# Optimization experiments

Measured on AMD Instinct MI355X. Metric: run time of the kernel, lower is better.

## Reference

```python
import jax, jax.numpy as jnp
import numpy as np
from jax import lax

B, N, C = 256, 256, 192
HEADS = 6
HD = C // HEADS
WIN = 16
AGENT = 49
POOL = 7            # int(agent_num ** 0.5)
SCALE = HD ** -0.5


def _pool_matrix(inn, out):
    # PyTorch AdaptiveAvgPool2d bin edges: start=floor(i*inn/out), end=ceil((i+1)*inn/out)
    P = np.zeros((out, inn), np.float32)
    for i in range(out):
        s = (i * inn) // out
        e = -(((-(i + 1)) * inn) // out)
        P[i, s:e] = 1.0 / (e - s)
    return jnp.asarray(P)

_P = _pool_matrix(WIN, POOL)  # (7, 16) adaptive-avg-pool operator


def _resize_bilinear(x, out_h, out_w):
    # matches F.interpolate(mode='bilinear', align_corners=False)
    H, W = x.shape[-2], x.shape[-1]
    def idx(out, inn):
        s = (jnp.arange(out, dtype=jnp.float32) + 0.5) * (inn / out) - 0.5
        s = jnp.maximum(s, 0.0)
        i0 = jnp.minimum(jnp.floor(s).astype(jnp.int32), inn - 1)
        i1 = jnp.minimum(i0 + 1, inn - 1)
        return i0, i1, s - i0.astype(jnp.float32)
    h0, h1, th = idx(out_h, H)
    w0, w1, tw = idx(out_w, W)
    xh = x[..., h0, :] * (1.0 - th)[:, None] + x[..., h1, :] * th[:, None]
    return xh[..., :, w0] * (1.0 - tw) + xh[..., :, w1] * tw


def setup_inputs() -> dict:
    key = jax.random.key(0)
    ks = jax.random.split(key, 18)
    lin = lambda k: jax.random.normal(k, (C, C), jnp.float32) * 0.02
    zc = jnp.zeros((C,), jnp.float32)
    tn = lambda k, shp: jax.random.normal(k, shp, jnp.float32) * 0.02
    return {
        "x_F1": jax.random.normal(ks[0], (B, N, C), jnp.float32),
        "x_C2": jax.random.normal(ks[1], (B, N, C), jnp.float32),
        "x_C1": jax.random.normal(ks[2], (B, N, C), jnp.float32),
        "Wq": lin(ks[3]), "bq": zc,
        "Wk": lin(ks[4]), "bk": zc,
        "Wv": lin(ks[5]), "bv": zc,
        "Wa1": lin(ks[6]), "ba1": zc,
        "Wa2": lin(ks[7]), "ba2": zc,
        "an_bias": tn(ks[8], (HEADS, AGENT, 7, 7)),
        "na_bias": tn(ks[9], (HEADS, AGENT, 7, 7)),
        "ah_bias": tn(ks[10], (1, HEADS, AGENT, WIN, 1)),
        "aw_bias": tn(ks[11], (1, HEADS, AGENT, 1, WIN)),
        "ha_bias": tn(ks[12], (1, HEADS, WIN, 1, AGENT)),
        "wa_bias": tn(ks[13], (1, HEADS, 1, WIN, AGENT)),
        "dwc_w": tn(ks[14], (C, 1, 3, 3)),
        "dwc_b": zc,
        "Wp": lin(ks[15]), "bp": zc,
    }


def reference(x_F1, x_C2, x_C1, Wq, bq, Wk, bk, Wv, bv, Wa1, ba1, Wa2, ba2,
              an_bias, na_bias, ah_bias, aw_bias, ha_bias, wa_bias,
              dwc_w, dwc_b, Wp, bp):
    b, n, c = x_F1.shape
    h = w = WIN
    q = x_F1 @ Wq.T + bq
    k = (x_F1 + x_C2 - x_C1) @ Wk.T + bk
    v = (x_C2 - x_C1) @ Wv.T + bv
    # agent tokens: linear -> adaptive avg pool 16x16 -> 7x7 -> (b, 49, c)
    a1 = (x_C1 @ Wa1.T + ba1).reshape(b, h, w, c)
    a1 = jnp.einsum('ph,bhwc,qw->bpqc', _P, a1, _P).reshape(b, AGENT, c)
    a2 = (x_C2 @ Wa2.T + ba2).reshape(b, h, w, c)
    a2 = jnp.einsum('ph,bhwc,qw->bpqc', _P, a2, _P).reshape(b, AGENT, c)
    qh = q.reshape(b, n, HEADS, HD).transpose(0, 2, 1, 3)
    kh = k.reshape(b, n, HEADS, HD).transpose(0, 2, 1, 3)
    vh = v.reshape(b, n, HEADS, HD).transpose(0, 2, 1, 3)
    a1h = a1.reshape(b, AGENT, HEADS, HD).transpose(0, 2, 1, 3)
    a2h = a2.reshape(b, AGENT, HEADS, HD).transpose(0, 2, 1, 3)
    # stage 1: agent <- k/v attention, bias = interp(an_bias) + (ah+aw)
    pb = (_resize_bilinear(an_bias, h, w).reshape(1, HEADS, AGENT, n)
          + (ah_bias + aw_bias).reshape(1, HEADS, AGENT, n))
    attn2 = jax.nn.softmax(SCALE * jnp.einsum('bhad,bhnd->bhan', a2h, kh) + pb, axis=-1)
    agent_v = jnp.einsum('bhan,bhnd->bhad', attn2, vh)
    # stage 2: query <- agent attention, bias = interp(na_bias)^T + (ha+wa)
    ab = (jnp.swapaxes(_resize_bilinear(na_bias, h, w).reshape(HEADS, AGENT, n), -1, -2)[None]
          + (ha_bias + wa_bias).reshape(1, HEADS, n, AGENT))
    q_attn = jax.nn.softmax(SCALE * jnp.einsum('bhnd,bhad->bhna', qh, a1h) + ab, axis=-1)
    x = jnp.einsum('bhna,bhad->bhnd', q_attn, agent_v).transpose(0, 2, 1, 3).reshape(b, n, c)
    # depthwise 3x3 conv on q as spatial map
    q_img = q.reshape(b, h, w, c).transpose(0, 3, 1, 2)
    dw = lax.conv_general_dilated(q_img, dwc_w, (1, 1), ((1, 1), (1, 1)),
                                  feature_group_count=c,
                                  dimension_numbers=('NCHW', 'OIHW', 'NCHW'))
    dw = dw + dwc_b.reshape(1, c, 1, 1)
    x = x + dw.transpose(0, 2, 3, 1).reshape(b, n, c)
    return x @ Wp.T + bp
```

## Files before the change

kernel.cpp:

```cpp
#include <hip/hip_runtime.h>

typedef __bf16 bf16;
typedef __bf16 bf16x4 __attribute__((ext_vector_type(4)));
typedef __bf16 bf16x8 __attribute__((ext_vector_type(8)));
typedef float  f32x4  __attribute__((ext_vector_type(4)));

#define DEVI __device__ __forceinline__

static constexpr int   BATCH = 256;
static constexpr int   SEQ   = 256;
static constexpr int   CH    = 192;
static constexpr int   NH    = 6;
static constexpr int   AG    = 49;
static constexpr float QK_SCALE = 0.17677669529663687f;

__device__ constexpr int   PPN[16]  = {1,1,2,1,2,1,2,1,1,2,1,2,1,2,1,1};
__device__ constexpr int   PPB0[16] = {0,0,0,1,1,2,2,3,3,3,4,4,5,5,6,6};
__device__ constexpr int   PPB1[16] = {0,0,1,0,2,0,3,0,0,4,0,5,0,6,0,0};
__device__ constexpr float PPW0[16] = {1.f/3.f,1.f/3.f,1.f/3.f,1.f/3.f,1.f/3.f,1.f/3.f,1.f/3.f,0.25f,0.25f,0.25f,
                                       1.f/3.f,1.f/3.f,1.f/3.f,1.f/3.f,1.f/3.f,1.f/3.f};
__device__ constexpr float PPW1[16] = {0.f,0.f,1.f/3.f,0.f,1.f/3.f,0.f,0.25f,0.f,0.f,1.f/3.f,
                                       0.f,1.f/3.f,0.f,1.f/3.f,0.f,0.f};

#if defined(__has_builtin)
#if __has_builtin(__builtin_amdgcn_global_load_lds)
#define HAVE_GLL 1
#endif
#endif

DEVI void gll16(const void* g, void* l, int lane) {
#ifdef HAVE_GLL
  (void)lane;
  __builtin_amdgcn_global_load_lds(
      (const __attribute__((address_space(1))) void*)g,
      (__attribute__((address_space(3))) void*)l, 16, 0, 0);
#else
  *(uint4*)((char*)l + lane * 16) = *(const uint4*)((const char*)g);
#endif
}

DEVI float bilin7(const float* m, int i, int j) {
  float sh = (i + 0.5f) * 0.4375f - 0.5f; sh = sh < 0.f ? 0.f : sh;
  float sw = (j + 0.5f) * 0.4375f - 0.5f; sw = sw < 0.f ? 0.f : sw;
  int i0 = (int)sh; if (i0 > 6) i0 = 6;
  int j0 = (int)sw; if (j0 > 6) j0 = 6;
  int i1 = i0 + 1;  if (i1 > 6) i1 = 6;
  int j1 = j0 + 1;  if (j1 > 6) j1 = 6;
  float th = sh - (float)i0, tw = sw - (float)j0;
  float v00 = m[i0*7 + j0], v01 = m[i0*7 + j1];
  float v10 = m[i1*7 + j0], v11 = m[i1*7 + j1];
  return (v00*(1.f-tw) + v01*tw)*(1.f-th) + (v10*(1.f-tw) + v11*tw)*th;
}

__global__ void k_prep(const float* Wq, const float* Wk, const float* Wv,
                       const float* Wa1, const float* Wa2, const float* Wp,
                       const float* an_bias, const float* na_bias,
                       const float* ah_bias, const float* aw_bias,
                       const float* ha_bias, const float* wa_bias,
                       bf16* wsW, bf16* pb, bf16* ab, bf16* a1, bf16* a2) {
  int gid = blockIdx.x * 256 + threadIdx.x;
  if (gid < 221184) {
    int mi = gid / 36864, r = gid - mi * 36864;
    const float* W = (mi == 0 ? Wq : mi == 1 ? Wk : mi == 2 ? Wv :
                      mi == 3 ? Wa1 : mi == 4 ? Wa2 : Wp);
    wsW[gid] = (bf16)W[r];
  } else if (gid < 296448) {
    int r = gid - 221184;
    int n = r & 255, ha = r >> 8;
    int i = n >> 4, j = n & 15;
    float val = bilin7(an_bias + (size_t)ha * 49, i, j)
              + ah_bias[ha * 16 + i] + aw_bias[ha * 16 + j];
    pb[r] = (bf16)val;
  } else if (gid < 382464) {
    int r = gid - 296448;
    int a = r % 56, hn = r / 56;
    int n = hn & 255, hh = hn >> 8;
    int i = n >> 4, j = n & 15;
    float val = 0.f;
    if (a < AG)
      val = bilin7(na_bias + (size_t)(hh * 49 + a) * 49, i, j)
          + ha_bias[(hh * 16 + i) * 49 + a] + wa_bias[(hh * 16 + j) * 49 + a];
    ab[r] = (bf16)val;
  } else if (gid < 407040) {
    int r = gid - 382464;
    if (r < 12288) a1[(size_t)12544 * CH + r] = (bf16)0.f;
    else           a2[(size_t)12544 * CH + (r - 12288)] = (bf16)0.f;
  }
}

__global__ __launch_bounds__(256, 4) void k_combo(
    const float* xF1, const float* xC2, const float* xC1,
    bf16* f1b, bf16* kin, bf16* vin) {
  const int base = blockIdx.x * 1536 + threadIdx.x;
  #pragma unroll
  for (int g = 0; g < 2; ++g) {
    int rows[3], byts[3];
    float f[3][8], c2[3][8], c1[3][8];
    #pragma unroll
    for (int s = 0; s < 3; ++s) {
      const int slot = base + 256 * (3 * g + s);
      const int row  = slot / 24;
      const int cb   = slot - row * 24;
      rows[s] = row;
      byts[s] = (cb * 16) ^ ((row & 7) << 4);
      const size_t rf = (size_t)row * CH + cb * 8;
      *(float4*)&f[s][0]  = *(const float4*)(xF1 + rf);
      *(float4*)&f[s][4]  = *(const float4*)(xF1 + rf + 4);
      *(float4*)&c2[s][0] = *(const float4*)(xC2 + rf);
      *(float4*)&c2[s][4] = *(const float4*)(xC2 + rf + 4);
      *(float4*)&c1[s][0] = *(const float4*)(xC1 + rf);
      *(float4*)&c1[s][4] = *(const float4*)(xC1 + rf + 4);
    }
    #pragma unroll
    for (int s = 0; s < 3; ++s) {
      bf16x8 tq, tk, tv;
      #pragma unroll
      for (int e = 0; e < 8; ++e) {
        const float d = c2[s][e] - c1[s][e];
        tq[e] = (bf16)f[s][e];
        tk[e] = (bf16)(f[s][e] + d);
        tv[e] = (bf16)d;
      }
      const size_t rowb = (size_t)rows[s] * 384;
      *(bf16x8*)((char*)f1b + rowb + byts[s]) = tq;
      *(bf16x8*)((char*)kin + rowb + byts[s]) = tk;
      *(bf16x8*)((char*)vin + rowb + byts[s]) = tv;
    }
  }
}

__global__ __launch_bounds__(256, 3) void k_gemm3b(
    const bf16* f1b, const bf16* kin, const bf16* vin, const bf16* wsW,
    const float* bq, const float* bk, const float* bv,
    bf16* qO, bf16* kO, bf16* vT) {
  __shared__ char sA[49152] __attribute__((aligned(16)));
  const int tid = threadIdx.x, lane = tid & 63, wid = tid >> 6;
  const int l15 = lane & 15, lg = lane >> 4;
  const int wr = wid >> 1, wc = wid & 1;
  const int job = blockIdx.y;
  const int m0 = blockIdx.x * 128;
  const bf16*  Aj   = (job == 0 ? f1b : job == 1 ? kin : vin);
  const bf16*  Wj   = wsW + job * 36864;
  const float* bias = (job == 0 ? bq : job == 1 ? bk : bv);

  {
    const char* gsrc = (const char*)Aj + (size_t)m0 * 384;
    #pragma unroll
    for (int i = 0; i < 12; ++i) {
      const int off = (wid * 12 + i) * 1024;
      gll16(gsrc + off + lane * 16, sA + off, lane);
    }
  }
  __syncthreads();

  f32x4 acc[4][6];
  #pragma unroll
  for (int a = 0; a < 4; ++a)
    #pragma unroll
    for (int b2 = 0; b2 < 6; ++b2) acc[a][b2] = f32x4{0.f, 0.f, 0.f, 0.f};

  #pragma unroll
  for (int kk = 0; kk < 6; ++kk) {
    bf16x8 af[4];
    #pragma unroll
    for (int rt = 0; rt < 4; ++rt) {
      const int row = 64 * wr + 16 * rt + l15;
      af[rt] = *(const bf16x8*)(sA + row * 384 + ((kk * 64 + lg * 16) ^ ((row & 7) << 4)));
    }
    #pragma unroll
    for (int ct = 0; ct < 6; ++ct) {
      const int ncol = 96 * wc + 16 * ct + l15;
      bf16x8 bfr = *(const bf16x8*)&Wj[(size_t)ncol * CH + kk * 32 + 8 * lg];
      #pragma unroll
      for (int rt = 0; rt < 4; ++rt)
        acc[rt][ct] = __builtin_amdgcn_mfma_f32_16x16x32_bf16(af[rt], bfr, acc[rt][ct], 0, 0, 0);
    }
  }
  __syncthreads();

  if (job < 2) {
    bf16* outp = (job == 0 ? qO : kO);
    #pragma unroll
    for (int ct = 0; ct < 6; ++ct) {
      const int col = 96 * wc + 16 * ct + l15;
      const float bb = bias[col];
      #pragma unroll
      for (int rt = 0; rt < 4; ++rt)
        #pragma unroll
        for (int r = 0; r < 4; ++r) {
          const int row = 64 * wr + 16 * rt + 4 * lg + r;
          *(bf16*)(sA + row * 384 + ((2 * col) ^ ((row & 7) << 4))) = (bf16)(acc[rt][ct][r] + bb);
        }
    }
    __syncthreads();
    #pragma unroll
    for (int g = 0; g < 12; ++g) {
      const int ch  = tid + 256 * g;
      const int row = ch / 24;
      const int y   = (ch - row * 24) * 16;
      bf16x8 vv = *(const bf16x8*)(sA + row * 384 + (y ^ ((row & 7) << 4)));
      *(bf16x8*)((char*)outp + (size_t)(m0 + row) * 384 + y) = vv;
    }
  } else {
    #pragma unroll
    for (int ct = 0; ct < 6; ++ct) {
      const int col = 96 * wc + 16 * ct + l15;
      const float bb = bias[col];
      #pragma unroll
      for (int rt = 0; rt < 4; ++rt)
        #pragma unroll
        for (int r = 0; r < 4; ++r) {
          const int row = 64 * wr + 16 * rt + 4 * lg + r;
          const int byt = col * 256 + (((2 * row) & ~15) ^ ((col & 7) << 4)) + ((2 * row) & 15);
          *(bf16*)(sA + byt) = (bf16)(acc[rt][ct][r] + bb);
        }
    }
    __syncthreads();
    const int batch = m0 >> 8, nb = m0 & 255;
    #pragma unroll
    for (int g = 0; g < 12; ++g) {
      const int ch = tid + 256 * g;
      const int c = ch >> 4, o = ch & 15;
      bf16x8 vv = *(const bf16x8*)(sA + c * 256 + ((o * 16) ^ ((c & 7) << 4)));
      *(bf16x8*)(vT + (((size_t)batch * NH + (c >> 5)) * 32 + (c & 31)) * 256 + nb + 8 * o) = vv;
    }
  }
}

#define POOLROW(I, P0, W0, P1, W1) do {                                        \
    float jqx[7] = {0,0,0,0,0,0,0}, jqy[7] = {0,0,0,0,0,0,0};                  \
    _Pragma("unroll")                                                          \
    for (int j = 0; j < 16; ++j) {                                             \
      float2 x = *(const float2*)(src + (size_t)((I) * 16 + j) * CH);          \
      jqx[PPB0[j]] += PPW0[j] * x.x;  jqy[PPB0[j]] += PPW0[j] * x.y;           \
      if (PPN[j] == 2) { jqx[PPB1[j]] += PPW1[j] * x.x;                        \
                         jqy[PPB1[j]] += PPW1[j] * x.y; }                      \
    }                                                                          \
    _Pragma("unroll")                                                          \
    for (int q = 0; q < 7; ++q) { ax[P0][q] += (W0) * jqx[q];                  \
                                  ay[P0][q] += (W0) * jqy[q]; }                \
    if ((P1) >= 0) {                                                           \
      _Pragma("unroll")                                                        \
      for (int q = 0; q < 7; ++q) { ax[(P1) & 3][q] += (W1) * jqx[q];          \
                                    ay[(P1) & 3][q] += (W1) * jqy[q]; }        \
    }                                                                          \
  } while (0)

__global__ __launch_bounds__(192) void k_pool(
    const float* xC1, const float* xC2, bf16* pooled1, bf16* pooled2) {
  __shared__ float lred[7][192];
  const int b = blockIdx.x, which = blockIdx.y, t = threadIdx.x;
  const int cp = t % 96, ih = t / 96;
  const float* src = (which ? xC2 : xC1) + (size_t)b * SEQ * CH + 2 * cp;
  bf16* dst = (which ? pooled2 : pooled1) + (size_t)b * AG * CH + 2 * cp;

  float ax[4][7], ay[4][7];
  #pragma unroll
  for (int p = 0; p < 4; ++p)
    #pragma unroll
    for (int q = 0; q < 7; ++q) { ax[p][q] = 0.f; ay[p][q] = 0.f; }

  const float TH = 1.f / 3.f, QU = 0.25f;
  if (ih == 0) {
    POOLROW(0, 0, TH, -1, 0.f);  POOLROW(1, 0, TH, -1, 0.f);
    POOLROW(2, 0, TH,  1, TH);   POOLROW(3, 1, TH, -1, 0.f);
    POOLROW(4, 1, TH,  2, TH);   POOLROW(5, 2, TH, -1, 0.f);
    POOLROW(6, 2, TH,  3, QU);   POOLROW(7, 3, QU, -1, 0.f);
  } else {
    POOLROW(8,  0, QU, -1, 0.f); POOLROW(9,  0, QU,  1, TH);
    POOLROW(10, 1, TH, -1, 0.f); POOLROW(11, 1, TH,  2, TH);
    POOLROW(12, 2, TH, -1, 0.f); POOLROW(13, 2, TH,  3, TH);
    POOLROW(14, 3, TH, -1, 0.f); POOLROW(15, 3, TH, -1, 0.f);
  }
  if (ih == 1) {
    #pragma unroll
    for (int q = 0; q < 7; ++q) {
      lred[q][2 * cp] = ax[0][q]; lred[q][2 * cp + 1] = ay[0][q];
    }
  }
  __syncthreads();
  if (ih == 0) {
    #pragma unroll
    for (int q = 0; q < 7; ++q) {
      ax[3][q] += lred[q][2 * cp]; ay[3][q] += lred[q][2 * cp + 1];
    }
    #pragma unroll
    for (int p = 0; p < 4; ++p)
      #pragma unroll
      for (int q = 0; q < 7; ++q) {
        union { bf16 e[2]; unsigned u; } u;
        u.e[0] = (bf16)ax[p][q]; u.e[1] = (bf16)ay[p][q];
        *(unsigned*)&dst[(size_t)(p * 7 + q) * CH] = u.u;
      }
  } else {
    #pragma unroll
    for (int lp = 1; lp < 4; ++lp)
      #pragma unroll
      for (int q = 0; q < 7; ++q) {
        union { bf16 e[2]; unsigned u; } u;
        u.e[0] = (bf16)ax[lp][q]; u.e[1] = (bf16)ay[lp][q];
        *(unsigned*)&dst[(size_t)((3 + lp) * 7 + q) * CH] = u.u;
      }
  }
}

DEVI void gemm_body(const bf16* Asrc, const bf16* W, const float* bias,
                    bf16* outp, int m0, bf16 (*sA)[72]) {
  const int tid = threadIdx.x, lane = tid & 63, wid = tid >> 6;
  const int l15 = lane & 15, lg = lane >> 4;
  const int wr = wid >> 1, wc = wid & 1;
  const int srow = tid >> 1, shalf = tid & 1;

  f32x4 acc[4][6];
  #pragma unroll
  for (int a = 0; a < 4; ++a)
    #pragma unroll
    for (int b2 = 0; b2 < 6; ++b2) acc[a][b2] = f32x4{0.f, 0.f, 0.f, 0.f};

  for (int ks = 0; ks < 3; ++ks) {
    const int k0 = ks * 64;
    const uint4* src = (const uint4*)(Asrc + (size_t)(m0 + srow) * CH + k0 + shalf * 32);
    #pragma unroll
    for (int i2 = 0; i2 < 4; ++i2)
      *(uint4*)&sA[srow][shalf * 32 + 8 * i2] = src[i2];
    __syncthreads();
    #pragma unroll
    for (int kk = 0; kk < 64; kk += 32) {
      bf16x8 af[4];
      #pragma unroll
      for (int rt = 0; rt < 4; ++rt)
        af[rt] = *(const bf16x8*)&sA[64 * wr + 16 * rt + l15][kk + 8 * lg];
      #pragma unroll
      for (int ct = 0; ct < 6; ++ct) {
        const int ncol = 96 * wc + 16 * ct + l15;
        bf16x8 bfr = *(const bf16x8*)&W[(size_t)ncol * CH + k0 + kk + 8 * lg];
        #pragma unroll
        for (int rt = 0; rt < 4; ++rt)
          acc[rt][ct] = __builtin_amdgcn_mfma_f32_16x16x32_bf16(af[rt], bfr, acc[rt][ct], 0, 0, 0);
      }
    }
    __syncthreads();
  }
  #pragma unroll
  for (int ct = 0; ct < 6; ++ct) {
    const int col = 96 * wc + 16 * ct + l15;
    const float bb = bias[col];
    #pragma unroll
    for (int rt = 0; rt < 4; ++rt) {
      const size_t rbase = (size_t)(m0 + 64 * wr + 16 * rt + 4 * lg);
      #pragma unroll
      for (int r = 0; r < 4; ++r)
        outp[(rbase + r) * CH + col] = (bf16)(acc[rt][ct][r] + bb);
    }
  }
}

__global__ __launch_bounds__(256, 2) void k_gemm2(
    const bf16* pooled1, const bf16* pooled2, const bf16* wsW,
    const float* ba1, const float* ba2, bf16* a1, bf16* a2) {
  __shared__ bf16 sA[128][72] __attribute__((aligned(16)));
  const int m0 = blockIdx.x * 128;
  if (blockIdx.y == 0) gemm_body(pooled1, wsW + 3 * 36864, ba1, a1, m0, sA);
  else                 gemm_body(pooled2, wsW + 4 * 36864, ba2, a2, m0, sA);
}

__global__ __launch_bounds__(256, 3) void k_gemm_out(
    const bf16* xsum, const bf16* Wp, const float* bp, float* out) {
  __shared__ char sA[49152] __attribute__((aligned(16)));
  const int tid = threadIdx.x, lane = tid & 63, wid = tid >> 6;
  const int l15 = lane & 15, lg = lane >> 4;
  const int wr = wid >> 1, wc = wid & 1;
  const int m0 = blockIdx.x * 128;

  {
    const char* gsrc = (const char*)xsum + (size_t)m0 * 384;
    #pragma unroll
    for (int i = 0; i < 12; ++i) {
      const int off = (wid * 12 + i) * 1024;
      gll16(gsrc + off + lane * 16, sA + off, lane);
    }
  }
  __syncthreads();

  f32x4 acc[4][6];
  #pragma unroll
  for (int a = 0; a < 4; ++a)
    #pragma unroll
    for (int b2 = 0; b2 < 6; ++b2) acc[a][b2] = f32x4{0.f, 0.f, 0.f, 0.f};

  #pragma unroll
  for (int kk = 0; kk < 6; ++kk) {
    bf16x8 af[4];
    #pragma unroll
    for (int rt = 0; rt < 4; ++rt) {
      const int row = 64 * wr + 16 * rt + l15;
      af[rt] = *(const bf16x8*)(sA + row * 384 + ((kk * 64 + lg * 16) ^ ((row & 7) << 4)));
    }
    #pragma unroll
    for (int ct = 0; ct < 6; ++ct) {
      const int ncol = 96 * wc + 16 * ct + l15;
      bf16x8 bfr = *(const bf16x8*)&Wp[(size_t)ncol * CH + kk * 32 + 8 * lg];
      #pragma unroll
      for (int rt = 0; rt < 4; ++rt)
        acc[rt][ct] = __builtin_amdgcn_mfma_f32_16x16x32_bf16(af[rt], bfr, acc[rt][ct], 0, 0, 0);
    }
  }
  #pragma unroll
  for (int ct = 0; ct < 6; ++ct) {
    const int col = 96 * wc + 16 * ct + l15;
    const float bb = bp[col];
    #pragma unroll
    for (int rt = 0; rt < 4; ++rt)
      #pragma unroll
      for (int r = 0; r < 4; ++r)
        out[(size_t)(m0 + 64 * wr + 16 * rt + 4 * lg + r) * CH + col] = acc[rt][ct][r] + bb;
  }
}

__global__ __launch_bounds__(256, 4) void k_attn(
    const bf16* q, const bf16* k, const bf16* vT,
    const bf16* a1, const bf16* a2, const bf16* pb, const bf16* ab,
    bf16* xattnH) {
  const int h = blockIdx.x, b = blockIdx.y;
  __shared__ char SM[39680] __attribute__((aligned(16)));
  bf16  (*log1)[264] = reinterpret_cast<bf16 (*)[264]>(SM);
  bf16  (*log2)[56]  = reinterpret_cast<bf16 (*)[56]>(SM);
  bf16  (*sAVT)[72]  = reinterpret_cast<bf16 (*)[72]>(SM + 33792);
  float* srow1       = reinterpret_cast<float*>(SM + 38400);
  float* srow2       = reinterpret_cast<float*>(SM + 38656);

  const int tid = threadIdx.x, lane = tid & 63, wv = tid >> 6;
  const int l15 = lane & 15, lg = lane >> 4;

  const bf16* qb  = q  + (size_t)b * SEQ * CH + h * 32;
  const bf16* kb  = k  + (size_t)b * SEQ * CH + h * 32;
  const bf16* vTb = vT + ((size_t)(b * NH + h) * 32) * 256;
  const bf16* a1b = a1 + (size_t)b * AG  * CH + h * 32;
  const bf16* a2b = a2 + (size_t)b * AG  * CH + h * 32;

  {
    bf16x8 afr[4];
    #pragma unroll
    for (int rt = 0; rt < 4; ++rt)
      afr[rt] = *(const bf16x8*)(a2b + (size_t)(16 * rt + l15) * CH + 8 * lg);
    #pragma unroll
    for (int ct = 0; ct < 4; ++ct) {
      const int n = 64 * wv + 16 * ct + l15;
      bf16x8 bfr = *(const bf16x8*)(kb + (size_t)n * CH + 8 * lg);
      #pragma unroll
      for (int rt = 0; rt < 4; ++rt) {
        f32x4 acc = {0.f, 0.f, 0.f, 0.f};
        acc = __builtin_amdgcn_mfma_f32_16x16x32_bf16(afr[rt], bfr, acc, 0, 0, 0);
        #pragma unroll
        for (int r = 0; r < 4; ++r)
          log1[16 * rt + 4 * lg + r][n] = (bf16)acc[r];
      }
    }
  }
  __syncthreads();

  if (tid < 196) {
    const int a = tid >> 2, qu = tid & 3;
    const bf16* pbrow = pb + ((size_t)h * AG + a) * SEQ + qu * 64;
    float m = -1e30f;
    #pragma unroll
    for (int i2 = 0; i2 < 8; ++i2) {
      bf16x8 raw = *(const bf16x8*)&log1[a][qu * 64 + 8 * i2];
      bf16x8 pbb = *(const bf16x8*)&pbrow[8 * i2];
      #pragma unroll
      for (int j = 0; j < 8; ++j)
        m = fmaxf(m, QK_SCALE * (float)raw[j] + (float)pbb[j]);
    }
    m = fmaxf(m, __shfl_xor(m, 1));
    m = fmaxf(m, __shfl_xor(m, 2));
    float s = 0.f;
    #pragma unroll
    for (int i2 = 0; i2 < 8; ++i2) {
      bf16x8 raw = *(const bf16x8*)&log1[a][qu * 64 + 8 * i2];
      bf16x8 pbb = *(const bf16x8*)&pbrow[8 * i2];
      bf16x8 eb;
      #pragma unroll
      for (int j = 0; j < 8; ++j) {
        float e = __expf(QK_SCALE * (float)raw[j] + (float)pbb[j] - m);
        s += e;
        eb[j] = (bf16)e;
      }
      *(bf16x8*)&log1[a][qu * 64 + 8 * i2] = eb;
    }
    s += __shfl_xor(s, 1);
    s += __shfl_xor(s, 2);
    if (qu == 0) srow1[a] = 1.f / s;
  }

  {
    f32x4 acc0 = {0.f, 0.f, 0.f, 0.f}, acc1 = {0.f, 0.f, 0.f, 0.f};
    #pragma unroll
    for (int ksn = 0; ksn < 8; ++ksn) {
      bf16x8 af = *(const bf16x8*)&log1[16 * wv + l15][32 * ksn + 8 * lg];
      bf16x8 b0 = *(const bf16x8*)(vTb + (size_t)l15 * 256 + 32 * ksn + 8 * lg);
      bf16x8 b1 = *(const bf16x8*)(vTb + (size_t)(16 + l15) * 256 + 32 * ksn + 8 * lg);
      acc0 = __builtin_amdgcn_mfma_f32_16x16x32_bf16(af, b0, acc0, 0, 0, 0);
      acc1 = __builtin_amdgcn_mfma_f32_16x16x32_bf16(af, b1, acc1, 0, 0, 0);
    }
    #pragma unroll
    for (int r = 0; r < 4; ++r) {
      const int a = 16 * wv + 4 * lg + r;
      const float inv = (a < AG) ? srow1[a] : 0.f;
      sAVT[l15][a]      = (bf16)(acc0[r] * inv);
      sAVT[16 + l15][a] = (bf16)(acc1[r] * inv);
    }
  }
  __syncthreads();

  {
    bf16x8 bfr[4];
    #pragma unroll
    for (int ct = 0; ct < 4; ++ct)
      bfr[ct] = *(const bf16x8*)(a1b + (size_t)(16 * ct + l15) * CH + 8 * lg);
    #pragma unroll
    for (int rt = 0; rt < 4; ++rt) {
      bf16x8 af = *(const bf16x8*)(qb + (size_t)(64 * wv + 16 * rt + l15) * CH + 8 * lg);
      #pragma unroll
      for (int ct = 0; ct < 4; ++ct) {
        f32x4 acc = {0.f, 0.f, 0.f, 0.f};
        acc = __builtin_amdgcn_mfma_f32_16x16x32_bf16(af, bfr[ct], acc, 0, 0, 0);
        if (ct < 3 || l15 == 0) {
          #pragma unroll
          for (int r = 0; r < 4; ++r)
            log2[64 * wv + 16 * rt + 4 * lg + r][16 * ct + l15] = (bf16)acc[r];
        }
      }
    }
  }

  {
    const bf16* abrow = ab + ((size_t)h * SEQ + tid) * 56;
    float m = -1e30f;
    #pragma unroll
    for (int i2 = 0; i2 < 6; ++i2) {
      bf16x8 raw = *(const bf16x8*)&log2[tid][8 * i2];
      bf16x8 abb = *(const bf16x8*)&abrow[8 * i2];
      #pragma unroll
      for (int j = 0; j < 8; ++j)
        m = fmaxf(m, QK_SCALE * (float)raw[j] + (float)abb[j]);
    }
    m = fmaxf(m, QK_SCALE * (float)log2[tid][48] + (float)abrow[48]);
    float s = 0.f;
    #pragma unroll
    for (int i2 = 0; i2 < 6; ++i2) {
      bf16x8 raw = *(const bf16x8*)&log2[tid][8 * i2];
      bf16x8 abb = *(const bf16x8*)&abrow[8 * i2];
      bf16x8 eb;
      #pragma unroll
      for (int j = 0; j < 8; ++j) {
        float e = __expf(QK_SCALE * (float)raw[j] + (float)abb[j] - m);
        s += e;
        eb[j] = (bf16)e;
      }
      *(bf16x8*)&log2[tid][8 * i2] = eb;
    }
    {
      float e48 = __expf(QK_SCALE * (float)log2[tid][48] + (float)abrow[48] - m);
      s += e48;
      bf16x8 eb;
      eb[0] = (bf16)e48;
      #pragma unroll
      for (int j = 1; j < 8; ++j) eb[j] = (bf16)0.f;
      *(bf16x8*)&log2[tid][48] = eb;
    }
    srow2[tid] = 1.f / s;
  }

  {
    bf16x8 bfr[2][2];
    #pragma unroll
    for (int ksn = 0; ksn < 2; ++ksn) {
      bfr[ksn][0] = *(const bf16x8*)&sAVT[l15][32 * ksn + 8 * lg];
      bfr[ksn][1] = *(const bf16x8*)&sAVT[16 + l15][32 * ksn + 8 * lg];
    }
    #pragma unroll
    for (int rt = 0; rt < 4; ++rt) {
      f32x4 acc0 = {0.f, 0.f, 0.f, 0.f}, acc1 = {0.f, 0.f, 0.f, 0.f};
      #pragma unroll
      for (int ksn = 0; ksn < 2; ++ksn) {
        bf16x8 af = *(const bf16x8*)&log2[64 * wv + 16 * rt + l15][32 * ksn + 8 * lg];
        acc0 = __builtin_amdgcn_mfma_f32_16x16x32_bf16(af, bfr[ksn][0], acc0, 0, 0, 0);
        acc1 = __builtin_amdgcn_mfma_f32_16x16x32_bf16(af, bfr[ksn][1], acc1, 0, 0, 0);
      }
      #pragma unroll
      for (int r = 0; r < 4; ++r) {
        const int nq = 64 * wv + 16 * rt + 4 * lg + r;
        const float inv = srow2[nq];
        log2[nq][l15]      = (bf16)(acc0[r] * inv);
        log2[nq][16 + l15] = (bf16)(acc1[r] * inv);
      }
    }
  }

  {
    bf16* dst = xattnH + ((size_t)(b * NH + h)) * SEQ * 32;
    #pragma unroll
    for (int u = 0; u < 4; ++u) {
      const int ch  = 256 * wv + 64 * u + lane;
      const int row = ch >> 2, qr = ch & 3;
      bf16x8 vv = *(const bf16x8*)&log2[row][8 * qr];
      *(bf16x8*)(dst + (size_t)ch * 8) = vv;
    }
  }
}

DEVI void fma8(float* acc, bf16x8 qv, float4 wa, float4 wb) {
  acc[0] += (float)qv[0] * wa.x; acc[1] += (float)qv[1] * wa.y;
  acc[2] += (float)qv[2] * wa.z; acc[3] += (float)qv[3] * wa.w;
  acc[4] += (float)qv[4] * wb.x; acc[5] += (float)qv[5] * wb.y;
  acc[6] += (float)qv[6] * wb.z; acc[7] += (float)qv[7] * wb.w;
}

__global__ __launch_bounds__(256) void k_dwconv(
    const bf16* q, const bf16* xattnH, const float* dwc_w, const float* dwc_b,
    bf16* xsum) {
  __shared__ bf16 sQ[144][200] __attribute__((aligned(16)));
  __shared__ float sW[9][192] __attribute__((aligned(16)));
  const int half = blockIdx.x, b = blockIdx.y;
  const int t = threadIdx.x;
  const int base_n = half ? 112 : 0;

  if (t < 144) {
    const bf16* qs = q + ((size_t)b * SEQ + base_n + t) * CH;
    #pragma unroll
    for (int i2 = 0; i2 < 24; ++i2)
      *(uint4*)&sQ[t][8 * i2] = ((const uint4*)qs)[i2];
  }
  for (int idx = t; idx < 9 * 192; idx += 256) {
    int cc = idx / 9, tap = idx - cc * 9;
    sW[tap][cc] = dwc_w[idx];
  }
  __syncthreads();

  const int nloc = t & 127, chalf = t >> 7;
  const int n = half * 128 + nloc;
  const int ii = n >> 4, jj = n & 15;
  const bf16* xaB = xattnH + (size_t)b * NH * SEQ * 32;
  char* xo = (char*)xsum + (size_t)(b * SEQ + n) * 384;
  const int sw = (n & 7) << 4;
  const int c_base = chalf * 96;

  for (int c0 = c_base; c0 < c_base + 96; c0 += 8) {
    float accv[8];
    {
      const float4* bsrc = (const float4*)(dwc_b + c0);
      float4 b0 = bsrc[0], b1 = bsrc[1];
      accv[0] = b0.x; accv[1] = b0.y; accv[2] = b0.z; accv[3] = b0.w;
      accv[4] = b1.x; accv[5] = b1.y; accv[6] = b1.z; accv[7] = b1.w;
    }
    {
      bf16x8 xv = *(const bf16x8*)(xaB + ((size_t)(c0 >> 5) * SEQ + n) * 32 + (c0 & 31));
      #pragma unroll
      for (int j = 0; j < 8; ++j) accv[j] += (float)xv[j];
    }
    #pragma unroll
    for (int di = 0; di < 3; ++di) {
      const int i2 = ii + di - 1;
      if ((unsigned)i2 >= 16u) continue;
      #pragma unroll
      for (int dj = 0; dj < 3; ++dj) {
        const int j2 = jj + dj - 1;
        if ((unsigned)j2 >= 16u) continue;
        const int nn = i2 * 16 + j2 - base_n;
        bf16x8 qv = *(const bf16x8*)&sQ[nn][c0];
        const float4* wv4 = (const float4*)&sW[di * 3 + dj][c0];
        fma8(accv, qv, wv4[0], wv4[1]);
      }
    }
    bf16x8 ob;
    #pragma unroll
    for (int j = 0; j < 8; ++j) ob[j] = (bf16)accv[j];
    *(bf16x8*)(xo + ((2 * c0) ^ sw)) = ob;
  }
}

extern "C" void kernel_launch(void* const* d_in, const int* in_sizes, int n_in,
                              void* d_out, int out_size, void* d_ws, size_t ws_size,
                              hipStream_t stream) {
  (void)in_sizes; (void)n_in; (void)out_size; (void)ws_size;
  const float* xF1 = (const float*)d_in[0];
  const float* xC2 = (const float*)d_in[1];
  const float* xC1 = (const float*)d_in[2];
  const float* Wq  = (const float*)d_in[3];
  const float* bq  = (const float*)d_in[4];
  const float* Wk  = (const float*)d_in[5];
  const float* bk  = (const float*)d_in[6];
  const float* Wv  = (const float*)d_in[7];
  const float* bv  = (const float*)d_in[8];
  const float* Wa1 = (const float*)d_in[9];
  const float* ba1 = (const float*)d_in[10];
  const float* Wa2 = (const float*)d_in[11];
  const float* ba2 = (const float*)d_in[12];
  const float* an_bias = (const float*)d_in[13];
  const float* na_bias = (const float*)d_in[14];
  const float* ah_bias = (const float*)d_in[15];
  const float* aw_bias = (const float*)d_in[16];
  const float* ha_bias = (const float*)d_in[17];
  const float* wa_bias = (const float*)d_in[18];
  const float* dwc_w = (const float*)d_in[19];
  const float* dwc_b = (const float*)d_in[20];
  const float* Wp  = (const float*)d_in[21];
  const float* bp  = (const float*)d_in[22];

  char* ws = (char*)d_ws;
  size_t off = 0;
  auto nxt = [&](size_t bytes) -> char* {
    char* p = ws + off;
    off = (off + bytes + 255) & ~(size_t)255;
    return p;
  };
  const size_t XSZ = (size_t)BATCH * SEQ * CH;
  const size_t ASZ = ((size_t)BATCH * AG + 64) * CH;

  bf16*  wsW     = (bf16*)nxt(6 * 36864 * sizeof(bf16));
  bf16*  pb      = (bf16*)nxt(6 * 49 * 256 * sizeof(bf16));
  bf16*  ab      = (bf16*)nxt(6 * 256 * 56 * sizeof(bf16));
  bf16*  pooled1 = (bf16*)nxt(ASZ * sizeof(bf16));
  bf16*  pooled2 = (bf16*)nxt(ASZ * sizeof(bf16));
  bf16*  f1b     = (bf16*)nxt(XSZ * sizeof(bf16));
  bf16*  kin     = (bf16*)nxt(XSZ * sizeof(bf16));
  bf16*  vin     = (bf16*)nxt(XSZ * sizeof(bf16));
  bf16*  qB      = (bf16*)nxt(XSZ * sizeof(bf16));
  bf16*  kB      = (bf16*)nxt(XSZ * sizeof(bf16));
  bf16*  vTB     = (bf16*)nxt(XSZ * sizeof(bf16));
  bf16*  a1B     = (bf16*)nxt(ASZ * sizeof(bf16));
  bf16*  a2B     = (bf16*)nxt(ASZ * sizeof(bf16));
  bf16*  xattnH  = f1b;
  bf16*  xsum    = kin;

  k_prep<<<1590, 256, 0, stream>>>(Wq, Wk, Wv, Wa1, Wa2, Wp,
                                   an_bias, na_bias, ah_bias, aw_bias,
                                   ha_bias, wa_bias, wsW, pb, ab, a1B, a2B);
  k_combo<<<1024, 256, 0, stream>>>(xF1, xC2, xC1, f1b, kin, vin);
  k_gemm3b<<<dim3(512, 3), 256, 0, stream>>>(f1b, kin, vin, wsW, bq, bk, bv, qB, kB, vTB);
  k_pool<<<dim3(BATCH, 2), 192, 0, stream>>>(xC1, xC2, pooled1, pooled2);
  k_gemm2<<<dim3(98, 2), 256, 0, stream>>>(pooled1, pooled2, wsW, ba1, ba2, a1B, a2B);
  k_attn<<<dim3(NH, BATCH), 256, 0, stream>>>(qB, kB, vTB, a1B, a2B, pb, ab, xattnH);
  k_dwconv<<<dim3(2, BATCH), 256, 0, stream>>>(qB, xattnH, dwc_w, dwc_b, xsum);
  k_gemm_out<<<512, 256, 0, stream>>>(xsum, wsW + 5 * 36864, bp, (float*)d_out);
}
```

Before: 238.8 us.

## Merge independent front-end kernels into two block-dispatched launches

Combines prep, combo and pool into one k_front kernel, and the QKV GEMM plus agent GEMMs into one k_mid kernel, dispatching each role by block index. This cuts the launch count from eight to five and lets independent work share a grid, reducing launch gaps and tail underutilisation. In exchange the merged kernels carry the register and LDS footprint of their largest branch, which can lower occupancy, and the pool branch now leaves 64 of its 256 threads idle.

```diff
diff --git a/kernel.cpp b/kernel.cpp
--- a/kernel.cpp
+++ b/kernel.cpp
@@ -50,181 +50,6 @@
   float v00 = m[i0*7 + j0], v01 = m[i0*7 + j1];
   float v10 = m[i1*7 + j0], v11 = m[i1*7 + j1];
   return (v00*(1.f-tw) + v01*tw)*(1.f-th) + (v10*(1.f-tw) + v11*tw)*th;
-}
-
-__global__ void k_prep(const float* Wq, const float* Wk, const float* Wv,
-                       const float* Wa1, const float* Wa2, const float* Wp,
-                       const float* an_bias, const float* na_bias,
-                       const float* ah_bias, const float* aw_bias,
-                       const float* ha_bias, const float* wa_bias,
-                       bf16* wsW, bf16* pb, bf16* ab, bf16* a1, bf16* a2) {
-  int gid = blockIdx.x * 256 + threadIdx.x;
-  if (gid < 221184) {
-    int mi = gid / 36864, r = gid - mi * 36864;
-    const float* W = (mi == 0 ? Wq : mi == 1 ? Wk : mi == 2 ? Wv :
-                      mi == 3 ? Wa1 : mi == 4 ? Wa2 : Wp);
-    wsW[gid] = (bf16)W[r];
-  } else if (gid < 296448) {
-    int r = gid - 221184;
-    int n = r & 255, ha = r >> 8;
-    int i = n >> 4, j = n & 15;
-    float val = bilin7(an_bias + (size_t)ha * 49, i, j)
-              + ah_bias[ha * 16 + i] + aw_bias[ha * 16 + j];
-    pb[r] = (bf16)val;
-  } else if (gid < 382464) {
-    int r = gid - 296448;
-    int a = r % 56, hn = r / 56;
-    int n = hn & 255, hh = hn >> 8;
-    int i = n >> 4, j = n & 15;
-    float val = 0.f;
-    if (a < AG)
-      val = bilin7(na_bias + (size_t)(hh * 49 + a) * 49, i, j)
-          + ha_bias[(hh * 16 + i) * 49 + a] + wa_bias[(hh * 16 + j) * 49 + a];
-    ab[r] = (bf16)val;
-  } else if (gid < 407040) {
-    int r = gid - 382464;
-    if (r < 12288) a1[(size_t)12544 * CH + r] = (bf16)0.f;
-    else           a2[(size_t)12544 * CH + (r - 12288)] = (bf16)0.f;
-  }
-}
-
-__global__ __launch_bounds__(256, 4) void k_combo(
-    const float* xF1, const float* xC2, const float* xC1,
-    bf16* f1b, bf16* kin, bf16* vin) {
-  const int base = blockIdx.x * 1536 + threadIdx.x;
-  #pragma unroll
-  for (int g = 0; g < 2; ++g) {
-    int rows[3], byts[3];
-    float f[3][8], c2[3][8], c1[3][8];
-    #pragma unroll
-    for (int s = 0; s < 3; ++s) {
-      const int slot = base + 256 * (3 * g + s);
-      const int row  = slot / 24;
-      const int cb   = slot - row * 24;
-      rows[s] = row;
-      byts[s] = (cb * 16) ^ ((row & 7) << 4);
-      const size_t rf = (size_t)row * CH + cb * 8;
-      *(float4*)&f[s][0]  = *(const float4*)(xF1 + rf);
-      *(float4*)&f[s][4]  = *(const float4*)(xF1 + rf + 4);
-      *(float4*)&c2[s][0] = *(const float4*)(xC2 + rf);
-      *(float4*)&c2[s][4] = *(const float4*)(xC2 + rf + 4);
-      *(float4*)&c1[s][0] = *(const float4*)(xC1 + rf);
-      *(float4*)&c1[s][4] = *(const float4*)(xC1 + rf + 4);
-    }
-    #pragma unroll
-    for (int s = 0; s < 3; ++s) {
-      bf16x8 tq, tk, tv;
-      #pragma unroll
-      for (int e = 0; e < 8; ++e) {
-        const float d = c2[s][e] - c1[s][e];
-        tq[e] = (bf16)f[s][e];
-        tk[e] = (bf16)(f[s][e] + d);
-        tv[e] = (bf16)d;
-      }
-      const size_t rowb = (size_t)rows[s] * 384;
-      *(bf16x8*)((char*)f1b + rowb + byts[s]) = tq;
-      *(bf16x8*)((char*)kin + rowb + byts[s]) = tk;
-      *(bf16x8*)((char*)vin + rowb + byts[s]) = tv;
-    }
-  }
-}
-
-__global__ __launch_bounds__(256, 3) void k_gemm3b(
-    const bf16* f1b, const bf16* kin, const bf16* vin, const bf16* wsW,
-    const float* bq, const float* bk, const float* bv,
-    bf16* qO, bf16* kO, bf16* vT) {
-  __shared__ char sA[49152] __attribute__((aligned(16)));
-  const int tid = threadIdx.x, lane = tid & 63, wid = tid >> 6;
-  const int l15 = lane & 15, lg = lane >> 4;
-  const int wr = wid >> 1, wc = wid & 1;
-  const int job = blockIdx.y;
-  const int m0 = blockIdx.x * 128;
-  const bf16*  Aj   = (job == 0 ? f1b : job == 1 ? kin : vin);
-  const bf16*  Wj   = wsW + job * 36864;
-  const float* bias = (job == 0 ? bq : job == 1 ? bk : bv);
-
-  {
-    const char* gsrc = (const char*)Aj + (size_t)m0 * 384;
-    #pragma unroll
-    for (int i = 0; i < 12; ++i) {
-      const int off = (wid * 12 + i) * 1024;
-      gll16(gsrc + off + lane * 16, sA + off, lane);
-    }
-  }
-  __syncthreads();
-
-  f32x4 acc[4][6];
-  #pragma unroll
-  for (int a = 0; a < 4; ++a)
-    #pragma unroll
-    for (int b2 = 0; b2 < 6; ++b2) acc[a][b2] = f32x4{0.f, 0.f, 0.f, 0.f};
-
-  #pragma unroll
-  for (int kk = 0; kk < 6; ++kk) {
-    bf16x8 af[4];
-    #pragma unroll
-    for (int rt = 0; rt < 4; ++rt) {
-      const int row = 64 * wr + 16 * rt + l15;
-      af[rt] = *(const bf16x8*)(sA + row * 384 + ((kk * 64 + lg * 16) ^ ((row & 7) << 4)));
-    }
-    #pragma unroll
-    for (int ct = 0; ct < 6; ++ct) {
-      const int ncol = 96 * wc + 16 * ct + l15;
-      bf16x8 bfr = *(const bf16x8*)&Wj[(size_t)ncol * CH + kk * 32 + 8 * lg];
-      #pragma unroll
-      for (int rt = 0; rt < 4; ++rt)
-        acc[rt][ct] = __builtin_amdgcn_mfma_f32_16x16x32_bf16(af[rt], bfr, acc[rt][ct], 0, 0, 0);
-    }
-  }
-  __syncthreads();
-
-  if (job < 2) {
-    bf16* outp = (job == 0 ? qO : kO);
-    #pragma unroll
-    for (int ct = 0; ct < 6; ++ct) {
-      const int col = 96 * wc + 16 * ct + l15;
-      const float bb = bias[col];
-      #pragma unroll
-      for (int rt = 0; rt < 4; ++rt)
-        #pragma unroll
-        for (int r = 0; r < 4; ++r) {
-          const int row = 64 * wr + 16 * rt + 4 * lg + r;
-          *(bf16*)(sA + row * 384 + ((2 * col) ^ ((row & 7) << 4))) = (bf16)(acc[rt][ct][r] + bb);
-        }
-    }
-    __syncthreads();
-    #pragma unroll
-    for (int g = 0; g < 12; ++g) {
-      const int ch  = tid + 256 * g;
-      const int row = ch / 24;
-      const int y   = (ch - row * 24) * 16;
-      bf16x8 vv = *(const bf16x8*)(sA + row * 384 + (y ^ ((row & 7) << 4)));
-      *(bf16x8*)((char*)outp + (size_t)(m0 + row) * 384 + y) = vv;
-    }
-  } else {
-    #pragma unroll
-    for (int ct = 0; ct < 6; ++ct) {
-      const int col = 96 * wc + 16 * ct + l15;
-      const float bb = bias[col];
-      #pragma unroll
-      for (int rt = 0; rt < 4; ++rt)
-        #pragma unroll
-        for (int r = 0; r < 4; ++r) {
-          const int row = 64 * wr + 16 * rt + 4 * lg + r;
-          const int byt = col * 256 + (((2 * row) & ~15) ^ ((col & 7) << 4)) + ((2 * row) & 15);
-          *(bf16*)(sA + byt) = (bf16)(acc[rt][ct][r] + bb);
-        }
-    }
-    __syncthreads();
-    const int batch = m0 >> 8, nb = m0 & 255;
-    #pragma unroll
-    for (int g = 0; g < 12; ++g) {
-      const int ch = tid + 256 * g;
-      const int c = ch >> 4, o = ch & 15;
-      bf16x8 vv = *(const bf16x8*)(sA + c * 256 + ((o * 16) ^ ((c & 7) << 4)));
-      *(bf16x8*)(vT + (((size_t)batch * NH + (c >> 5)) * 32 + (c & 31)) * 256 + nb + 8 * o) = vv;
-    }
-  }
 }
 
 #define POOLROW(I, P0, W0, P1, W1) do {                                        \
@@ -246,61 +71,146 @@
     }                                                                          \
   } while (0)
 
-__global__ __launch_bounds__(192) void k_pool(
-    const float* xC1, const float* xC2, bf16* pooled1, bf16* pooled2) {
+__global__ __launch_bounds__(256, 2) void k_front(
+    const float* xF1, const float* xC2, const float* xC1,
+    const float* Wq, const float* Wk, const float* Wv,
+    const float* Wa1, const float* Wa2, const float* Wp,
+    const float* an_bias, const float* na_bias,
+    const float* ah_bias, const float* aw_bias,
+    const float* ha_bias, const float* wa_bias,
+    bf16* f1b, bf16* kin, bf16* vin,
+    bf16* pooled1, bf16* pooled2,
+    bf16* wsW, bf16* pb, bf16* ab, bf16* a1, bf16* a2) {
   __shared__ float lred[7][192];
-  const int b = blockIdx.x, which = blockIdx.y, t = threadIdx.x;
-  const int cp = t % 96, ih = t / 96;
-  const float* src = (which ? xC2 : xC1) + (size_t)b * SEQ * CH + 2 * cp;
-  bf16* dst = (which ? pooled2 : pooled1) + (size_t)b * AG * CH + 2 * cp;
-
-  float ax[4][7], ay[4][7];
-  #pragma unroll
-  for (int p = 0; p < 4; ++p)
-    #pragma unroll
-    for (int q = 0; q < 7; ++q) { ax[p][q] = 0.f; ay[p][q] = 0.f; }
-
-  const float TH = 1.f / 3.f, QU = 0.25f;
-  if (ih == 0) {
-    POOLROW(0, 0, TH, -1, 0.f);  POOLROW(1, 0, TH, -1, 0.f);
-    POOLROW(2, 0, TH,  1, TH);   POOLROW(3, 1, TH, -1, 0.f);
-    POOLROW(4, 1, TH,  2, TH);   POOLROW(5, 2, TH, -1, 0.f);
-    POOLROW(6, 2, TH,  3, QU);   POOLROW(7, 3, QU, -1, 0.f);
+  const int bx = blockIdx.x;
+
+  if (bx < 1024) {
+    const int base = bx * 1536 + threadIdx.x;
+    #pragma unroll
+    for (int g = 0; g < 2; ++g) {
+      int rows[3], byts[3];
+      float f[3][8], c2[3][8], c1[3][8];
+      #pragma unroll
+      for (int s = 0; s < 3; ++s) {
+        const int slot = base + 256 * (3 * g + s);
+        const int row  = slot / 24;
+        const int cb   = slot - row * 24;
+        rows[s] = row;
+        byts[s] = (cb * 16) ^ ((row & 7) << 4);
+        const size_t rf = (size_t)row * CH + cb * 8;
+        *(float4*)&f[s][0]  = *(const float4*)(xF1 + rf);
+        *(float4*)&f[s][4]  = *(const float4*)(xF1 + rf + 4);
+        *(float4*)&c2[s][0] = *(const float4*)(xC2 + rf);
+        *(float4*)&c2[s][4] = *(const float4*)(xC2 + rf + 4);
+        *(float4*)&c1[s][0] = *(const float4*)(xC1 + rf);
+        *(float4*)&c1[s][4] = *(const float4*)(xC1 + rf + 4);
+      }
+      #pragma unroll
+      for (int s = 0; s < 3; ++s) {
+        bf16x8 tq, tk, tv;
+        #pragma unroll
+        for (int e = 0; e < 8; ++e) {
+          const float d = c2[s][e] - c1[s][e];
+          tq[e] = (bf16)f[s][e];
+          tk[e] = (bf16)(f[s][e] + d);
+          tv[e] = (bf16)d;
+        }
+        const size_t rowb = (size_t)rows[s] * 384;
+        *(bf16x8*)((char*)f1b + rowb + byts[s]) = tq;
+        *(bf16x8*)((char*)kin + rowb + byts[s]) = tk;
+        *(bf16x8*)((char*)vin + rowb + byts[s]) = tv;
+      }
+    }
+  } else if (bx < 1536) {
+    const int idx = bx - 1024;
+    const int b = idx & 255, which = idx >> 8;
+    const int t = threadIdx.x;
+    const int cp = (t < 192) ? (t % 96) : 0;
+    const int ih = (t < 192) ? (t / 96) : 0;
+    const float* src = (which ? xC2 : xC1) + (size_t)b * SEQ * CH + 2 * cp;
+    bf16* dst = (which ? pooled2 : pooled1) + (size_t)b * AG * CH + 2 * cp;
+
+    float ax[4][7], ay[4][7];
+    #pragma unroll
+    for (int p = 0; p < 4; ++p)
+      #pragma unroll
+      for (int q = 0; q < 7; ++q) { ax[p][q] = 0.f; ay[p][q] = 0.f; }
+
+    const float TH = 1.f / 3.f, QU = 0.25f;
+    if (t < 192) {
+      if (ih == 0) {
+        POOLROW(0, 0, TH, -1, 0.f);  POOLROW(1, 0, TH, -1, 0.f);
+        POOLROW(2, 0, TH,  1, TH);   POOLROW(3, 1, TH, -1, 0.f);
+        POOLROW(4, 1, TH,  2, TH);   POOLROW(5, 2, TH, -1, 0.f);
+        POOLROW(6, 2, TH,  3, QU);   POOLROW(7, 3, QU, -1, 0.f);
+      } else {
+        POOLROW(8,  0, QU, -1, 0.f); POOLROW(9,  0, QU,  1, TH);
+        POOLROW(10, 1, TH, -1, 0.f); POOLROW(11, 1, TH,  2, TH);
+        POOLROW(12, 2, TH, -1, 0.f); POOLROW(13, 2, TH,  3, TH);
+        POOLROW(14, 3, TH, -1, 0.f); POOLROW(15, 3, TH, -1, 0.f);
+      }
+      if (ih == 1) {
+        #pragma unroll
+        for (int q = 0; q < 7; ++q) {
+          lred[q][2 * cp] = ax[0][q]; lred[q][2 * cp + 1] = ay[0][q];
+        }
+      }
+    }
+    __syncthreads();
+    if (t < 192) {
+      if (ih == 0) {
+        #pragma unroll
+        for (int q = 0; q < 7; ++q) {
+          ax[3][q] += lred[q][2 * cp]; ay[3][q] += lred[q][2 * cp + 1];
+        }
+        #pragma unroll
+        for (int p = 0; p < 4; ++p)
+          #pragma unroll
+          for (int q = 0; q < 7; ++q) {
+            union { bf16 e[2]; unsigned u; } u;
+            u.e[0] = (bf16)ax[p][q]; u.e[1] = (bf16)ay[p][q];
+            *(unsigned*)&dst[(size_t)(p * 7 + q) * CH] = u.u;
+          }
+      } else {
+        #pragma unroll
+        for (int lp = 1; lp < 4; ++lp)
+          #pragma unroll
+          for (int q = 0; q < 7; ++q) {
+            union { bf16 e[2]; unsigned u; } u;
+            u.e[0] = (bf16)ax[lp][q]; u.e[1] = (bf16)ay[lp][q];
+            *(unsigned*)&dst[(size_t)((3 + lp) * 7 + q) * CH] = u.u;
+          }
+      }
+    }
   } else {
-    POOLROW(8,  0, QU, -1, 0.f); POOLROW(9,  0, QU,  1, TH);
-    POOLROW(10, 1, TH, -1, 0.f); POOLROW(11, 1, TH,  2, TH);
-    POOLROW(12, 2, TH, -1, 0.f); POOLROW(13, 2, TH,  3, TH);
-    POOLROW(14, 3, TH, -1, 0.f); POOLROW(15, 3, TH, -1, 0.f);
-  }
-  if (ih == 1) {
-    #pragma unroll
-    for (int q = 0; q < 7; ++q) {
-      lred[q][2 * cp] = ax[0][q]; lred[q][2 * cp + 1] = ay[0][q];
-    }
-  }
-  __syncthreads();
-  if (ih == 0) {
-    #pragma unroll
-    for (int q = 0; q < 7; ++q) {
-      ax[3][q] += lred[q][2 * cp]; ay[3][q] += lred[q][2 * cp + 1];
-    }
-    #pragma unroll
-    for (int p = 0; p < 4; ++p)
-      #pragma unroll
-      for (int q = 0; q < 7; ++q) {
-        union { bf16 e[2]; unsigned u; } u;
-        u.e[0] = (bf16)ax[p][q]; u.e[1] = (bf16)ay[p][q];
-        *(unsigned*)&dst[(size_t)(p * 7 + q) * CH] = u.u;
-      }
-  } else {
-    #pragma unroll
-    for (int lp = 1; lp < 4; ++lp)
-      #pragma unroll
-      for (int q = 0; q < 7; ++q) {
-        union { bf16 e[2]; unsigned u; } u;
-        u.e[0] = (bf16)ax[lp][q]; u.e[1] = (bf16)ay[lp][q];
-        *(unsigned*)&dst[(size_t)((3 + lp) * 7 + q) * CH] = u.u;
-      }
+    const int gid = (bx - 1536) * 256 + threadIdx.x;
+    if (gid < 221184) {
+      int mi = gid / 36864, r = gid - mi * 36864;
+      const float* W = (mi == 0 ? Wq : mi == 1 ? Wk : mi == 2 ? Wv :
+                        mi == 3 ? Wa1 : mi == 4 ? Wa2 : Wp);
+      wsW[gid] = (bf16)W[r];
+    } else if (gid < 296448) {
+      int r = gid - 221184;
+      int n = r & 255, ha = r >> 8;
+      int i = n >> 4, j = n & 15;
+      float val = bilin7(an_bias + (size_t)ha * 49, i, j)
+                + ah_bias[ha * 16 + i] + aw_bias[ha * 16 + j];
+      pb[r] = (bf16)val;
+    } else if (gid < 382464) {
+      int r = gid - 296448;
+      int a = r % 56, hn = r / 56;
+      int n = hn & 255, hh = hn >> 8;
+      int i = n >> 4, j = n & 15;
+      float val = 0.f;
+      if (a < AG)
+        val = bilin7(na_bias + (size_t)(hh * 49 + a) * 49, i, j)
+            + ha_bias[(hh * 16 + i) * 49 + a] + wa_bias[(hh * 16 + j) * 49 + a];
+      ab[r] = (bf16)val;
+    } else if (gid < 407040) {
+      int r = gid - 382464;
+      if (r < 12288) a1[(size_t)12544 * CH + r] = (bf16)0.f;
+      else           a2[(size_t)12544 * CH + (r - 12288)] = (bf16)0.f;
+    }
   }
 }
 
@@ -355,25 +265,36 @@
   }
 }
 
-__global__ __launch_bounds__(256, 2) void k_gemm2(
-    const bf16* pooled1, const bf16* pooled2, const bf16* wsW,
-    const float* ba1, const float* ba2, bf16* a1, bf16* a2) {
-  __shared__ bf16 sA[128][72] __attribute__((aligned(16)));
-  const int m0 = blockIdx.x * 128;
-  if (blockIdx.y == 0) gemm_body(pooled1, wsW + 3 * 36864, ba1, a1, m0, sA);
-  else                 gemm_body(pooled2, wsW + 4 * 36864, ba2, a2, m0, sA);
-}
-
-__global__ __launch_bounds__(256, 3) void k_gemm_out(
-    const bf16* xsum, const bf16* Wp, const float* bp, float* out) {
+__global__ __launch_bounds__(256, 3) void k_mid(
+    const bf16* f1b, const bf16* kin, const bf16* vin, const bf16* wsW,
+    const float* bq, const float* bk, const float* bv,
+    const bf16* pooled1, const bf16* pooled2,
+    const float* ba1, const float* ba2,
+    bf16* qO, bf16* kO, bf16* vT, bf16* a1, bf16* a2) {
   __shared__ char sA[49152] __attribute__((aligned(16)));
+  const int bx = blockIdx.x;
+
+  if (bx >= 1536) {
+    const int idx = bx - 1536;
+    const int m0 = (idx % 98) * 128;
+    if (idx < 98) gemm_body(pooled1, wsW + 3 * 36864, ba1, a1, m0,
+                            reinterpret_cast<bf16 (*)[72]>(sA));
+    else          gemm_body(pooled2, wsW + 4 * 36864, ba2, a2, m0,
+                            reinterpret_cast<bf16 (*)[72]>(sA));
+    return;
+  }
+
   const int tid = threadIdx.x, lane = tid & 63, wid = tid >> 6;
   const int l15 = lane & 15, lg = lane >> 4;
   const int wr = wid >> 1, wc = wid & 1;
-  const int m0 = blockIdx.x * 128;
+  const int job = bx >> 9;
+  const int m0 = (bx & 511) * 128;
+  const bf16*  Aj   = (job == 0 ? f1b : job == 1 ? kin : vin);
+  const bf16*  Wj   = wsW + job * 36864;
+  const float* bias = (job == 0 ? bq : job == 1 ? bk : bv);
 
   {
-    const char* gsrc = (const char*)xsum + (size_t)m0 * 384;
+    const char* gsrc = (const char*)Aj + (size_t)m0 * 384;
     #pragma unroll
     for (int i = 0; i < 12; ++i) {
       const int off = (wid * 12 + i) * 1024;
@@ -399,21 +320,60 @@
     #pragma unroll
     for (int ct = 0; ct < 6; ++ct) {
       const int ncol = 96 * wc + 16 * ct + l15;
-      bf16x8 bfr = *(const bf16x8*)&Wp[(size_t)ncol * CH + kk * 32 + 8 * lg];
+      bf16x8 bfr = *(const bf16x8*)&Wj[(size_t)ncol * CH + kk * 32 + 8 * lg];
       #pragma unroll
       for (int rt = 0; rt < 4; ++rt)
         acc[rt][ct] = __builtin_amdgcn_mfma_f32_16x16x32_bf16(af[rt], bfr, acc[rt][ct], 0, 0, 0);
     }
   }
-  #pragma unroll
-  for (int ct = 0; ct < 6; ++ct) {
-    const int col = 96 * wc + 16 * ct + l15;
-    const float bb = bp[col];
-    #pragma unroll
-    for (int rt = 0; rt < 4; ++rt)
-      #pragma unroll
-      for (int r = 0; r < 4; ++r)
-        out[(size_t)(m0 + 64 * wr + 16 * rt + 4 * lg + r) * CH + col] = acc[rt][ct][r] + bb;
+  __syncthreads();
+
+  if (job < 2) {
+    bf16* outp = (job == 0 ? qO : kO);
+    #pragma unroll
+    for (int ct = 0; ct < 6; ++ct) {
+      const int col = 96 * wc + 16 * ct + l15;
+      const float bb = bias[col];
+      #pragma unroll
+      for (int rt = 0; rt < 4; ++rt)
+        #pragma unroll
+        for (int r = 0; r < 4; ++r) {
+          const int row = 64 * wr + 16 * rt + 4 * lg + r;
+          *(bf16*)(sA + row * 384 + ((2 * col) ^ ((row & 7) << 4))) = (bf16)(acc[rt][ct][r] + bb);
+        }
+    }
+    __syncthreads();
+    #pragma unroll
+    for (int g = 0; g < 12; ++g) {
+      const int ch  = tid + 256 * g;
+      const int row = ch / 24;
+      const int y   = (ch - row * 24) * 16;
+      bf16x8 vv = *(const bf16x8*)(sA + row * 384 + (y ^ ((row & 7) << 4)));
+      *(bf16x8*)((char*)outp + (size_t)(m0 + row) * 384 + y) = vv;
+    }
+  } else {
+    #pragma unroll
+    for (int ct = 0; ct < 6; ++ct) {
+      const int col = 96 * wc + 16 * ct + l15;
+      const float bb = bias[col];
+      #pragma unroll
+      for (int rt = 0; rt < 4; ++rt)
+        #pragma unroll
+        for (int r = 0; r < 4; ++r) {
+          const int row = 64 * wr + 16 * rt + 4 * lg + r;
+          const int byt = col * 256 + (((2 * row) & ~15) ^ ((col & 7) << 4)) + ((2 * row) & 15);
+          *(bf16*)(sA + byt) = (bf16)(acc[rt][ct][r] + bb);
+        }
+    }
+    __syncthreads();
+    const int batch = m0 >> 8, nb = m0 & 255;
+    #pragma unroll
+    for (int g = 0; g < 12; ++g) {
+      const int ch = tid + 256 * g;
+      const int c = ch >> 4, o = ch & 15;
+      bf16x8 vv = *(const bf16x8*)(sA + c * 256 + ((o * 16) ^ ((c & 7) << 4)));
+      *(bf16x8*)(vT + (((size_t)batch * NH + (c >> 5)) * 32 + (c & 31)) * 256 + nb + 8 * o) = vv;
+    }
   }
 }
 
@@ -676,6 +636,59 @@
     #pragma unroll
     for (int j = 0; j < 8; ++j) ob[j] = (bf16)accv[j];
     *(bf16x8*)(xo + ((2 * c0) ^ sw)) = ob;
+  }
+}
+
+__global__ __launch_bounds__(256, 3) void k_gemm_out(
+    const bf16* xsum, const bf16* Wp, const float* bp, float* out) {
+  __shared__ char sA[49152] __attribute__((aligned(16)));
+  const int tid = threadIdx.x, lane = tid & 63, wid = tid >> 6;
+  const int l15 = lane & 15, lg = lane >> 4;
+  const int wr = wid >> 1, wc = wid & 1;
+  const int m0 = blockIdx.x * 128;
+
+  {
+    const char* gsrc = (const char*)xsum + (size_t)m0 * 384;
+    #pragma unroll
+    for (int i = 0; i < 12; ++i) {
+      const int off = (wid * 12 + i) * 1024;
+      gll16(gsrc + off + lane * 16, sA + off, lane);
+    }
+  }
+  __syncthreads();
+
+  f32x4 acc[4][6];
+  #pragma unroll
+  for (int a = 0; a < 4; ++a)
+    #pragma unroll
+    for (int b2 = 0; b2 < 6; ++b2) acc[a][b2] = f32x4{0.f, 0.f, 0.f, 0.f};
+
+  #pragma unroll
+  for (int kk = 0; kk < 6; ++kk) {
+    bf16x8 af[4];
+    #pragma unroll
+    for (int rt = 0; rt < 4; ++rt) {
+      const int row = 64 * wr + 16 * rt + l15;
+      af[rt] = *(const bf16x8*)(sA + row * 384 + ((kk * 64 + lg * 16) ^ ((row & 7) << 4)));
+    }
+    #pragma unroll
+    for (int ct = 0; ct < 6; ++ct) {
+      const int ncol = 96 * wc + 16 * ct + l15;
+      bf16x8 bfr = *(const bf16x8*)&Wp[(size_t)ncol * CH + kk * 32 + 8 * lg];
+      #pragma unroll
+      for (int rt = 0; rt < 4; ++rt)
+        acc[rt][ct] = __builtin_amdgcn_mfma_f32_16x16x32_bf16(af[rt], bfr, acc[rt][ct], 0, 0, 0);
+    }
+  }
+  #pragma unroll
+  for (int ct = 0; ct < 6; ++ct) {
+    const int col = 96 * wc + 16 * ct + l15;
+    const float bb = bp[col];
+    #pragma unroll
+    for (int rt = 0; rt < 4; ++rt)
+      #pragma unroll
+      for (int r = 0; r < 4; ++r)
+        out[(size_t)(m0 + 64 * wr + 16 * rt + 4 * lg + r) * CH + col] = acc[rt][ct][r] + bb;
   }
 }
 
@@ -733,13 +746,15 @@
   bf16*  xattnH  = f1b;
   bf16*  xsum    = kin;
 
-  k_prep<<<1590, 256, 0, stream>>>(Wq, Wk, Wv, Wa1, Wa2, Wp,
-                                   an_bias, na_bias, ah_bias, aw_bias,
-                                   ha_bias, wa_bias, wsW, pb, ab, a1B, a2B);
-  k_combo<<<1024, 256, 0, stream>>>(xF1, xC2, xC1, f1b, kin, vin);
-  k_gemm3b<<<dim3(512, 3), 256, 0, stream>>>(f1b, kin, vin, wsW, bq, bk, bv, qB, kB, vTB);
-  k_pool<<<dim3(BATCH, 2), 192, 0, stream>>>(xC1, xC2, pooled1, pooled2);
-  k_gemm2<<<dim3(98, 2), 256, 0, stream>>>(pooled1, pooled2, wsW, ba1, ba2, a1B, a2B);
+  k_front<<<3126, 256, 0, stream>>>(xF1, xC2, xC1,
+                                    Wq, Wk, Wv, Wa1, Wa2, Wp,
+                                    an_bias, na_bias, ah_bias, aw_bias,
+                                    ha_bias, wa_bias,
+                                    f1b, kin, vin, pooled1, pooled2,
+                                    wsW, pb, ab, a1B, a2B);
+  k_mid<<<1732, 256, 0, stream>>>(f1b, kin, vin, wsW, bq, bk, bv,
+                                  pooled1, pooled2, ba1, ba2,
+                                  qB, kB, vTB, a1B, a2B);
   k_attn<<<dim3(NH, BATCH), 256, 0, stream>>>(qB, kB, vTB, a1B, a2B, pb, ab, xattnH);
   k_dwconv<<<dim3(2, BATCH), 256, 0, stream>>>(qB, xattnH, dwc_w, dwc_b, xsum);
   k_gemm_out<<<512, 256, 0, stream>>>(xsum, wsW + 5 * 36864, bp, (float*)d_out);
```

After: 231.1 us. 3.2% less time.
